# Kernel optimization log

Hardware: AMD Instinct MI355X
Metric: run time of the kernel (lower is better)

Reference implementation:

```python
import jax, jax.numpy as jnp
import numpy as np

N_NODE = 4_000_000
N_DOMAIN = 100_000


def setup_inputs() -> dict:
    key = jax.random.key(0)
    k1, k2, k3, k4 = jax.random.split(key, 4)
    pos = jax.random.normal(k1, (N_NODE, 3), dtype=jnp.float32)
    axes = jax.random.normal(k2, (N_DOMAIN, 3), dtype=jnp.float32)
    angles = jax.random.uniform(k3, (N_DOMAIN,), dtype=jnp.float32) * jnp.float32(np.pi)
    domain_index = jnp.sort(jax.random.randint(k4, (N_NODE,), 0, N_DOMAIN, dtype=jnp.int32)).astype(jnp.int64)
    node_index = jnp.arange(N_NODE, dtype=jnp.int64)
    return {
        "pos": pos,
        "axes": axes,
        "angles": angles,
        "domain_index": domain_index,
        "node_index": node_index,
        "n_domain": N_DOMAIN,
    }


def reference(pos, axes, angles, domain_index, node_index, n_domain):
    # Normalized rotation axes (matches F.normalize in _sample_axis)
    k = axes / jnp.linalg.norm(axes, axis=-1, keepdims=True)

    pg = pos[node_index]  # [n_node_domain, 3] gathered positions
    # scatter_mean over domains
    sums = jax.ops.segment_sum(pg, domain_index, num_segments=n_domain)
    counts = jax.ops.segment_sum(jnp.ones((pg.shape[0],), pg.dtype), domain_index, num_segments=n_domain)
    centers = sums / jnp.maximum(counts, 1.0)[:, None]  # [n_domain, 3]

    c_g = centers[domain_index]  # gathered centers per edge
    rel = pg - c_g
    kd = k[domain_index]
    ang = angles[domain_index]
    cos_t = jnp.cos(ang)[:, None]
    sin_t = jnp.sin(ang)[:, None]
    # Rodrigues: v cos t + (k x v) sin t + k (k.v)(1 - cos t)
    cross = jnp.cross(kd, rel)
    dot = jnp.sum(kd * rel, axis=-1, keepdims=True)
    rot = rel * cos_t + cross * sin_t + kd * dot * (1.0 - cos_t)

    pos_update = rot + c_g
    return pos.at[node_index].set(pos_update)
```

## Files before the change

kernel.cpp:

```cpp
#include <hip/hip_runtime.h>


#define BLK 256
#define LPD 32
#define DPB (BLK / LPD)

struct f3 { float x, y, z; };

__global__ __launch_bounds__(BLK) void rp_scatter_kernel(
    const int* __restrict__ dom,
    int2* __restrict__ se,
    long long nE)
{
    long long t = (long long)blockIdx.x * BLK + threadIdx.x;
    long long base = t * 4;
    if (base >= nE) return;
    if (base + 4 <= nE) {
        int4 dd = *(const int4*)(dom + base);
        if (base == 0) {
            se[dd.x].x = 0;
        } else {
            int dp = dom[base - 1];
            if (dp != dd.x) { se[dp].y = (int)base; se[dd.x].x = (int)base; }
        }
        if (dd.x != dd.y) { se[dd.x].y = (int)base + 1; se[dd.y].x = (int)base + 1; }
        if (dd.y != dd.z) { se[dd.y].y = (int)base + 2; se[dd.z].x = (int)base + 2; }
        if (dd.z != dd.w) { se[dd.z].y = (int)base + 3; se[dd.w].x = (int)base + 3; }
        if (base + 4 == nE) se[dd.w].y = (int)nE;
    } else {
        for (long long j = base; j < nE; ++j) {
            int d = dom[j];
            if (j == 0) {
                se[d].x = 0;
            } else {
                int dp = dom[j - 1];
                if (dp != d) { se[dp].y = (int)j; se[d].x = (int)j; }
            }
            if (j == nE - 1) se[d].y = (int)nE;
        }
    }
}

__global__ __launch_bounds__(BLK) void rp_fused_kernel(
    const f3* __restrict__ pos,
    const float* __restrict__ axes,
    const float* __restrict__ angles,
    const int2* __restrict__ se,
    f3* __restrict__ out,
    int nD, int nE)
{
    int d = blockIdx.x * DPB + (threadIdx.x >> 5);
    if (d >= nD) return;
    int sub = threadIdx.x & 31;
    int2 r = se[d];
    int s = r.x, e = r.y;
    if (s < 0 || e <= s || s >= nE || e > nE) return;

    int j0 = s + sub;
    int j1 = j0 + LPD;
    f3 c0, c1;
    float sx = 0.f, sy = 0.f, sz = 0.f;
    bool v0 = (j0 < e), v1 = (j1 < e);
    if (v0) { c0 = pos[j0]; sx += c0.x; sy += c0.y; sz += c0.z; }
    if (v1) { c1 = pos[j1]; sx += c1.x; sy += c1.y; sz += c1.z; }
    for (int j = j0 + 2 * LPD; j < e; j += LPD) {
        f3 p = pos[j];
        sx += p.x; sy += p.y; sz += p.z;
    }

    #pragma unroll
    for (int off = 1; off < LPD; off <<= 1) {
        sx += __shfl_xor(sx, off);
        sy += __shfl_xor(sy, off);
        sz += __shfl_xor(sz, off);
    }

    float inv_cnt = 1.0f / (float)(e - s);
    float cx = sx * inv_cnt, cy = sy * inv_cnt, cz = sz * inv_cnt;

    float kx = axes[(long long)d * 3 + 0];
    float ky = axes[(long long)d * 3 + 1];
    float kz = axes[(long long)d * 3 + 2];
    float invn = 1.0f / sqrtf(kx * kx + ky * ky + kz * kz);
    kx *= invn; ky *= invn; kz *= invn;
    float a = angles[d];
    float co = __cosf(a);
    float sn = __sinf(a);
    float omc = 1.0f - co;

    if (v0) {
        float rx = c0.x - cx, ry = c0.y - cy, rz = c0.z - cz;
        float crx = ky * rz - kz * ry;
        float cry = kz * rx - kx * rz;
        float crz = kx * ry - ky * rx;
        float dt = kx * rx + ky * ry + kz * rz;
        float tt = dt * omc;
        f3 o;
        o.x = rx * co + crx * sn + kx * tt + cx;
        o.y = ry * co + cry * sn + ky * tt + cy;
        o.z = rz * co + crz * sn + kz * tt + cz;
        out[j0] = o;
    }
    if (v1) {
        float rx = c1.x - cx, ry = c1.y - cy, rz = c1.z - cz;
        float crx = ky * rz - kz * ry;
        float cry = kz * rx - kx * rz;
        float crz = kx * ry - ky * rx;
        float dt = kx * rx + ky * ry + kz * rz;
        float tt = dt * omc;
        f3 o;
        o.x = rx * co + crx * sn + kx * tt + cx;
        o.y = ry * co + cry * sn + ky * tt + cy;
        o.z = rz * co + crz * sn + kz * tt + cz;
        out[j1] = o;
    }
    for (int j = j0 + 2 * LPD; j < e; j += LPD) {
        f3 p = pos[j];
        float rx = p.x - cx, ry = p.y - cy, rz = p.z - cz;
        float crx = ky * rz - kz * ry;
        float cry = kz * rx - kx * rz;
        float crz = kx * ry - ky * rx;
        float dt = kx * rx + ky * ry + kz * rz;
        float tt = dt * omc;
        f3 o;
        o.x = rx * co + crx * sn + kx * tt + cx;
        o.y = ry * co + cry * sn + ky * tt + cy;
        o.z = rz * co + crz * sn + kz * tt + cz;
        out[j] = o;
    }
}

extern "C" void kernel_launch(void* const* d_in, const int* in_sizes, int n_in,
                              void* d_out, int out_size, void* d_ws, size_t ws_size,
                              hipStream_t stream) {
    const float* posf   = (const float*)d_in[0];
    const float* axes   = (const float*)d_in[1];
    const float* angles = (const float*)d_in[2];
    const int*   dom    = (const int*)d_in[3];

    const int nD = in_sizes[2];
    const long long nE = in_sizes[3];

    int2* se = (int2*)d_ws;

    {
        long long nT = (nE + 3) / 4;
        long long grid = (nT + BLK - 1) / BLK;
        rp_scatter_kernel<<<(int)grid, BLK, 0, stream>>>(dom, se, nE);
    }
    {
        int grid = (nD + DPB - 1) / DPB;
        rp_fused_kernel<<<grid, BLK, 0, stream>>>((const f3*)posf, axes, angles,
                                                  se, (f3*)d_out, nD, (int)nE);
    }
}
```

Baseline: 30.60 us.

## Stage block's contiguous position range through shared memory with float4 loads/stores

```diff
diff --git a/kernel.cpp b/kernel.cpp
--- a/kernel.cpp
+++ b/kernel.cpp
@@ -4,6 +4,7 @@
 #define BLK 256
 #define LPD 32
 #define DPB (BLK / LPD)
+#define CAPP 768
 
 struct f3 { float x, y, z; };
 
@@ -43,90 +44,137 @@
 
 __global__ __launch_bounds__(BLK) void rp_fused_kernel(
     const f3* __restrict__ pos,
+    const float* __restrict__ posf,
     const float* __restrict__ axes,
     const float* __restrict__ angles,
     const int2* __restrict__ se,
     f3* __restrict__ out,
+    float* __restrict__ outf,
     int nD, int nE)
 {
-    int d = blockIdx.x * DPB + (threadIdx.x >> 5);
-    if (d >= nD) return;
-    int sub = threadIdx.x & 31;
-    int2 r = se[d];
-    int s = r.x, e = r.y;
-    if (s < 0 || e <= s || s >= nE || e > nE) return;
-
-    int j0 = s + sub;
-    int j1 = j0 + LPD;
-    f3 c0, c1;
-    float sx = 0.f, sy = 0.f, sz = 0.f;
-    bool v0 = (j0 < e), v1 = (j1 < e);
-    if (v0) { c0 = pos[j0]; sx += c0.x; sy += c0.y; sz += c0.z; }
-    if (v1) { c1 = pos[j1]; sx += c1.x; sy += c1.y; sz += c1.z; }
-    for (int j = j0 + 2 * LPD; j < e; j += LPD) {
-        f3 p = pos[j];
-        sx += p.x; sy += p.y; sz += p.z;
-    }
-
-    #pragma unroll
-    for (int off = 1; off < LPD; off <<= 1) {
-        sx += __shfl_xor(sx, off);
-        sy += __shfl_xor(sy, off);
-        sz += __shfl_xor(sz, off);
-    }
-
-    float inv_cnt = 1.0f / (float)(e - s);
-    float cx = sx * inv_cnt, cy = sy * inv_cnt, cz = sz * inv_cnt;
-
-    float kx = axes[(long long)d * 3 + 0];
-    float ky = axes[(long long)d * 3 + 1];
-    float kz = axes[(long long)d * 3 + 2];
-    float invn = 1.0f / sqrtf(kx * kx + ky * ky + kz * kz);
-    kx *= invn; ky *= invn; kz *= invn;
-    float a = angles[d];
-    float co = __cosf(a);
-    float sn = __sinf(a);
-    float omc = 1.0f - co;
-
-    if (v0) {
-        float rx = c0.x - cx, ry = c0.y - cy, rz = c0.z - cz;
-        float crx = ky * rz - kz * ry;
-        float cry = kz * rx - kx * rz;
-        float crz = kx * ry - ky * rx;
-        float dt = kx * rx + ky * ry + kz * rz;
-        float tt = dt * omc;
-        f3 o;
-        o.x = rx * co + crx * sn + kx * tt + cx;
-        o.y = ry * co + cry * sn + ky * tt + cy;
-        o.z = rz * co + crz * sn + kz * tt + cz;
-        out[j0] = o;
-    }
-    if (v1) {
-        float rx = c1.x - cx, ry = c1.y - cy, rz = c1.z - cz;
-        float crx = ky * rz - kz * ry;
-        float cry = kz * rx - kx * rz;
-        float crz = kx * ry - ky * rx;
-        float dt = kx * rx + ky * ry + kz * rz;
-        float tt = dt * omc;
-        f3 o;
-        o.x = rx * co + crx * sn + kx * tt + cx;
-        o.y = ry * co + cry * sn + ky * tt + cy;
-        o.z = rz * co + crz * sn + kz * tt + cz;
-        out[j1] = o;
-    }
-    for (int j = j0 + 2 * LPD; j < e; j += LPD) {
-        f3 p = pos[j];
-        float rx = p.x - cx, ry = p.y - cy, rz = p.z - cz;
-        float crx = ky * rz - kz * ry;
-        float cry = kz * rx - kx * rz;
-        float crz = kx * ry - ky * rx;
-        float dt = kx * rx + ky * ry + kz * rz;
-        float tt = dt * omc;
-        f3 o;
-        o.x = rx * co + crx * sn + kx * tt + cx;
-        o.y = ry * co + cry * sn + ky * tt + cy;
-        o.z = rz * co + crz * sn + kz * tt + cz;
-        out[j] = o;
+    __shared__ __align__(16) float lin[3 * CAPP + 4];
+    __shared__ __align__(16) float lout[3 * CAPP + 4];
+
+    const int tid = threadIdx.x;
+    const int d0 = blockIdx.x * DPB;
+    int dmaxp1 = d0 + DPB; if (dmaxp1 > nD) dmaxp1 = nD;
+    const int dmax = dmaxp1 - 1;
+
+    const int ps = se[d0].x;
+    const int pe = se[dmax].y;
+    const int nF = 3 * nE;
+    const int f0 = 3 * ps, f1 = 3 * pe;
+    const int a0 = f0 & ~3;
+    const bool staged = (ps >= 0) && (pe > ps) && (pe <= nE) &&
+                        (pe - ps <= CAPP);
+
+    if (staged) {
+        for (int idx = a0 + 4 * tid; idx < f1; idx += 4 * BLK) {
+            if (idx + 4 <= nF) {
+                *(float4*)(lin + (idx - a0)) = *(const float4*)(posf + idx);
+            } else {
+                #pragma unroll
+                for (int c = 0; c < 4; ++c)
+                    if (idx + c < nF) lin[idx - a0 + c] = posf[idx + c];
+            }
+        }
+        __syncthreads();
+    }
+
+    const int d = d0 + (tid >> 5);
+    const int sub = tid & 31;
+    bool gv = (d <= dmax);
+    int s = 0, e = 0;
+    if (gv) {
+        int2 r = se[d];
+        s = r.x; e = r.y;
+        gv = (s >= 0) && (e > s) && (e <= nE) &&
+             (!staged || (s >= ps && e <= pe));
+    }
+    if (gv) {
+        int j0 = s + sub;
+        int j1 = j0 + LPD;
+        bool v0 = (j0 < e), v1 = (j1 < e);
+        f3 c0, c1;
+        float sx = 0.f, sy = 0.f, sz = 0.f;
+        if (staged) {
+            if (v0) { int li = 3 * j0 - a0; c0 = { lin[li], lin[li + 1], lin[li + 2] };
+                      sx += c0.x; sy += c0.y; sz += c0.z; }
+            if (v1) { int li = 3 * j1 - a0; c1 = { lin[li], lin[li + 1], lin[li + 2] };
+                      sx += c1.x; sy += c1.y; sz += c1.z; }
+            for (int j = j0 + 2 * LPD; j < e; j += LPD) {
+                int li = 3 * j - a0;
+                sx += lin[li]; sy += lin[li + 1]; sz += lin[li + 2];
+            }
+        } else {
+            if (v0) { c0 = pos[j0]; sx += c0.x; sy += c0.y; sz += c0.z; }
+            if (v1) { c1 = pos[j1]; sx += c1.x; sy += c1.y; sz += c1.z; }
+            for (int j = j0 + 2 * LPD; j < e; j += LPD) {
+                f3 p = pos[j];
+                sx += p.x; sy += p.y; sz += p.z;
+            }
+        }
+
+        #pragma unroll
+        for (int off = 1; off < LPD; off <<= 1) {
+            sx += __shfl_xor(sx, off);
+            sy += __shfl_xor(sy, off);
+            sz += __shfl_xor(sz, off);
+        }
+
+        float inv_cnt = 1.0f / (float)(e - s);
+        float cx = sx * inv_cnt, cy = sy * inv_cnt, cz = sz * inv_cnt;
+
+        float kx = axes[(long long)d * 3 + 0];
+        float ky = axes[(long long)d * 3 + 1];
+        float kz = axes[(long long)d * 3 + 2];
+        float invn = 1.0f / sqrtf(kx * kx + ky * ky + kz * kz);
+        kx *= invn; ky *= invn; kz *= invn;
+        float a = angles[d];
+        float co = __cosf(a);
+        float sn = __sinf(a);
+        float omc = 1.0f - co;
+
+        #define ROT(P, OX, OY, OZ)                                   \
+            { float rx = (P).x - cx, ry = (P).y - cy, rz = (P).z - cz; \
+              float crx = ky * rz - kz * ry;                          \
+              float cry = kz * rx - kx * rz;                          \
+              float crz = kx * ry - ky * rx;                          \
+              float dt = kx * rx + ky * ry + kz * rz;                 \
+              float tt = dt * omc;                                    \
+              OX = rx * co + crx * sn + kx * tt + cx;                 \
+              OY = ry * co + cry * sn + ky * tt + cy;                 \
+              OZ = rz * co + crz * sn + kz * tt + cz; }
+
+        if (staged) {
+            if (v0) { int li = 3 * j0 - a0;
+                      ROT(c0, lout[li], lout[li + 1], lout[li + 2]); }
+            if (v1) { int li = 3 * j1 - a0;
+                      ROT(c1, lout[li], lout[li + 1], lout[li + 2]); }
+            for (int j = j0 + 2 * LPD; j < e; j += LPD) {
+                int li = 3 * j - a0;
+                f3 p = { lin[li], lin[li + 1], lin[li + 2] };
+                ROT(p, lout[li], lout[li + 1], lout[li + 2]);
+            }
+        } else {
+            if (v0) { f3 o; ROT(c0, o.x, o.y, o.z); out[j0] = o; }
+            if (v1) { f3 o; ROT(c1, o.x, o.y, o.z); out[j1] = o; }
+            for (int j = j0 + 2 * LPD; j < e; j += LPD) {
+                f3 p = pos[j];
+                f3 o; ROT(p, o.x, o.y, o.z); out[j] = o;
+            }
+        }
+        #undef ROT
+    }
+
+    if (staged) {
+        __syncthreads();
+        int h1 = (f0 + 3) & ~3; if (h1 > f1) h1 = f1;
+        int b1 = f1 & ~3;       if (b1 < h1) b1 = h1;
+        if (tid < h1 - f0) outf[f0 + tid] = lout[f0 + tid - a0];
+        for (int idx = h1 + 4 * tid; idx < b1; idx += 4 * BLK)
+            *(float4*)(outf + idx) = *(float4*)(lout + (idx - a0));
+        if (tid < f1 - b1) outf[b1 + tid] = lout[b1 + tid - a0];
     }
 }
 
@@ -150,7 +198,9 @@
     }
     {
         int grid = (nD + DPB - 1) / DPB;
-        rp_fused_kernel<<<grid, BLK, 0, stream>>>((const f3*)posf, axes, angles,
-                                                  se, (f3*)d_out, nD, (int)nE);
+        rp_fused_kernel<<<grid, BLK, 0, stream>>>((const f3*)posf, posf,
+                                                  axes, angles, se,
+                                                  (f3*)d_out, (float*)d_out,
+                                                  nD, (int)nE);
     }
 }
```

Result: slower. 40.39 us (+32.0%).
